# Performance work log

Hardware: AMD Instinct MI355X
Metric: run time of the kernel (lower is better)

Reference implementation:

```python
import jax, jax.numpy as jnp
import numpy as np

N = 100_000      # nodes
E = 1_600_000    # edges (before self-loops)
IN_C = 500
HID = 128
OUT_C = 64
L = 8
ALPHA = 0.1
THETA = 0.5


def setup_inputs() -> dict:
    key = jax.random.key(0)
    ks = jax.random.split(key, 6)
    x = jax.random.normal(ks[0], (N, IN_C), dtype=jnp.float32)
    edge_index = jax.random.randint(ks[1], (2, E), 0, N, dtype=jnp.int32)
    s0 = 1.0 / np.sqrt(IN_C)
    W_in = jax.random.uniform(ks[2], (IN_C, HID), jnp.float32, -s0, s0)
    b_in = jnp.zeros((HID,), jnp.float32)
    sh = 1.0 / np.sqrt(HID)
    W_conv = jax.random.uniform(ks[3], (L, HID, HID), jnp.float32, -sh, sh)
    W_out = jax.random.uniform(ks[4], (HID, OUT_C), jnp.float32, -sh, sh)
    b_out = jnp.zeros((OUT_C,), jnp.float32)
    return {"x": x, "edge_index": edge_index, "W_in": W_in, "b_in": b_in,
            "W_conv": W_conv, "W_out": W_out, "b_out": b_out}


def reference(x, edge_index, W_in, b_in, W_conv, W_out, b_out):
    # dropout is identity in eval mode
    loop = jnp.arange(N, dtype=edge_index.dtype)
    src = jnp.concatenate([edge_index[0], loop])  # add self-loops (gcn_norm)
    dst = jnp.concatenate([edge_index[1], loop])
    deg = jax.ops.segment_sum(jnp.ones_like(src, dtype=x.dtype), dst, num_segments=N)
    dinv = jnp.where(deg > 0, jax.lax.rsqrt(deg), 0.0)
    norm = dinv[src] * dinv[dst]  # symmetric normalization coeffs per edge

    h = jax.nn.relu(x @ W_in + b_in)
    h0 = h  # initial residual
    for l in range(L):
        beta = float(np.log(THETA / (l + 1) + 1.0))
        agg = jax.ops.segment_sum(h[src] * norm[:, None], dst, num_segments=N)  # Ahat @ h
        z = (1.0 - ALPHA) * agg + ALPHA * h0
        h = jax.nn.relu((1.0 - beta) * z + beta * (z @ W_conv[l]))
    return h @ W_out + b_out
```

## Files before the change

kernel.cpp:

```cpp
#include <hip/hip_runtime.h>
#include <hip/hip_fp16.h>
#include <cmath>

#define NN 100000
#define EE 1600000
#define INC 500
#define HIDC 128
#define OUTC 64
#define NLAYER 8
#define NW32 3125
#define GEMM_BLKS 782
#define FILL_BLKS 6250
#define FUSE_BLKS 7032

typedef float f32x4 __attribute__((ext_vector_type(4)));
typedef __bf16 bf16x8 __attribute__((ext_vector_type(8)));
typedef _Float16 f16x8 __attribute__((ext_vector_type(8)));
typedef short s16x4 __attribute__((ext_vector_type(4)));
typedef short s16x8 __attribute__((ext_vector_type(8)));

__device__ __forceinline__ unsigned short f2bf_rn(float f) {
  unsigned u = __float_as_uint(f);
  unsigned r = u + 0x7fffu + ((u >> 16) & 1u);
  return (unsigned short)(r >> 16);
}
__device__ __forceinline__ float bf2f(unsigned short h) {
  return __uint_as_float(((unsigned)h) << 16);
}

__device__ __forceinline__ int fraddr(int row, int k, int Kp) {
  return (row >> 4) * (Kp * 16) + (k >> 3) * 128 + (row & 15) * 8 + (k & 7);
}


__global__ void k_count_deg(const int* __restrict__ dst, int* __restrict__ deg, int E) {
  int e = blockIdx.x * blockDim.x + threadIdx.x;
  if (e < E) atomicAdd(&deg[dst[e]], 1);
}

__global__ void k_scan_block_sums(const int* __restrict__ deg, int* __restrict__ bsum, int n) {
  __shared__ int sm[256];
  int i = blockIdx.x * 256 + threadIdx.x;
  int v = (i < n) ? deg[i] + 1 : 0;
  sm[threadIdx.x] = v;
  __syncthreads();
  for (int s = 128; s > 0; s >>= 1) {
    if (threadIdx.x < s) sm[threadIdx.x] += sm[threadIdx.x + s];
    __syncthreads();
  }
  if (threadIdx.x == 0) bsum[blockIdx.x] = sm[0];
}

__global__ void k_scan_partials(int* __restrict__ bsum, int nb) {
  __shared__ int sm[512];
  int t = threadIdx.x;
  sm[t] = (t < nb) ? bsum[t] : 0;
  __syncthreads();
  for (int s = 1; s < 512; s <<= 1) {
    int v = (t >= s) ? sm[t - s] : 0;
    __syncthreads();
    sm[t] += v;
    __syncthreads();
  }
  if (t < nb) bsum[t] = (t == 0) ? 0 : sm[t - 1];
}

__global__ void k_scan_final(const int* __restrict__ deg, const int* __restrict__ bsum,
                             int* __restrict__ row_ptr, int n) {
  __shared__ int sm[256];
  int i = blockIdx.x * 256 + threadIdx.x;
  int v = (i < n) ? deg[i] + 1 : 0;
  sm[threadIdx.x] = v;
  __syncthreads();
  for (int s = 1; s < 256; s <<= 1) {
    int u = (threadIdx.x >= s) ? sm[threadIdx.x - s] : 0;
    __syncthreads();
    sm[threadIdx.x] += u;
    __syncthreads();
  }
  if (i < n) row_ptr[i] = bsum[blockIdx.x] + sm[threadIdx.x] - v;
}

__global__ void k_init_rows(const int* __restrict__ deg, const int* __restrict__ row_ptr,
                            int* __restrict__ cursor, int* __restrict__ col,
                            float* __restrict__ dinv, int n) {
  int i = blockIdx.x * blockDim.x + threadIdx.x;
  if (i < n) {
    int rp = row_ptr[i];
    col[rp] = i;
    cursor[i] = rp + 1;
    dinv[i] = rsqrtf((float)(deg[i] + 1));
  }
}


__global__ void k_prep_wfin(const float* __restrict__ W, unsigned short* __restrict__ fh,
                            unsigned short* __restrict__ fl) {
  int i = blockIdx.x * 256 + threadIdx.x;
  if (i >= HIDC * 512) return;
  int n = i / 512, k = i % 512;
  float v = (k < INC) ? W[(size_t)k * HIDC + n] : 0.f;
  unsigned short h = f2bf_rn(v);
  unsigned short l = f2bf_rn(v - bf2f(h));
  int a = fraddr(n, k, 512);
  fh[a] = h;
  fl[a] = l;
}


__global__ void k_prep_wf16(const float* __restrict__ W, __half* __restrict__ f,
                            int K, int N, float idc, float ws) {
  int i = blockIdx.x * 256 + threadIdx.x;
  if (i >= N * K) return;
  int n = i / K, k = i % K;
  float v = ws * W[(size_t)k * N + n] + ((k == n) ? idc : 0.f);
  f[fraddr(n, k, K)] = __float2half(v);
}


__global__ void __launch_bounds__(256) k_fill_gemm(
    const int* __restrict__ src, const int* __restrict__ dst,
    int* __restrict__ cursor, int* __restrict__ col,
    const float* __restrict__ A, const unsigned short* __restrict__ Bfh,
    const unsigned short* __restrict__ Bfl, const float* __restrict__ bias,
    __half* __restrict__ C16u, __half* __restrict__ C16s,
    const float* __restrict__ dinv) {
  __shared__ __align__(16) unsigned short Ah[128 * 40];
  __shared__ __align__(16) unsigned short Al[128 * 40];
  int bid = blockIdx.x;
  int tid = threadIdx.x;

  if (bid % 9 != 0) {
    int fidx = bid - (bid / 9 + 1);
    int e = fidx * 256 + tid;
    if (e < EE) {
      int pos = atomicAdd(&cursor[dst[e]], 1);
      col[pos] = src[e];
    }
    return;
  }

  int blk = bid / 9;
  int wid = tid >> 6, lane = tid & 63;
  int wr = wid >> 1, wc = wid & 1;
  int lr = lane & 15, kg = lane >> 4;
  int row0 = blk * 128;

  f32x4 acc[4][4];
#pragma unroll
  for (int m = 0; m < 4; ++m)
#pragma unroll
    for (int n = 0; n < 4; ++n) acc[m][n] = {0.f, 0.f, 0.f, 0.f};

  float4 va[4];
  auto issue_loads = [&](int kt) {
#pragma unroll
    for (int p = 0; p < 4; ++p) {
      int idx = tid + p * 256;
      int r = idx >> 3, kq = idx & 7;
      int gr = row0 + r, gk = kt + kq * 4;
      va[p] = make_float4(0.f, 0.f, 0.f, 0.f);
      if (gr < NN && gk < INC) va[p] = *reinterpret_cast<const float4*>(&A[(size_t)gr * INC + gk]);
    }
  };

  issue_loads(0);
  for (int kt = 0; kt < 512; kt += 32) {
#pragma unroll
    for (int p = 0; p < 4; ++p) {
      int idx = tid + p * 256;
      int r = idx >> 3, kq = idx & 7;
      const float* vp = &va[p].x;
      s16x4 h4, l4;
#pragma unroll
      for (int e = 0; e < 4; ++e) {
        unsigned short h = f2bf_rn(vp[e]);
        h4[e] = (short)h;
        l4[e] = (short)f2bf_rn(vp[e] - bf2f(h));
      }
      *reinterpret_cast<s16x4*>(&Ah[r * 40 + kq * 4]) = h4;
      *reinterpret_cast<s16x4*>(&Al[r * 40 + kq * 4]) = l4;
    }
    __syncthreads();
    if (kt + 32 < 512) issue_loads(kt + 32);

    bf16x8 afh[4], afl[4];
#pragma unroll
    for (int m = 0; m < 4; ++m) {
      int r = wr * 64 + m * 16 + lr;
      afh[m] = *reinterpret_cast<const bf16x8*>(&Ah[r * 40 + kg * 8]);
      afl[m] = *reinterpret_cast<const bf16x8*>(&Al[r * 40 + kg * 8]);
    }
#pragma unroll
    for (int n = 0; n < 4; ++n) {
      size_t bb = (size_t)(wc * 4 + n) * 8192 + (size_t)(kt / 8 + kg) * 128 + lr * 8;
      bf16x8 bh = *reinterpret_cast<const bf16x8*>(&Bfh[bb]);
      bf16x8 bl = *reinterpret_cast<const bf16x8*>(&Bfl[bb]);
#pragma unroll
      for (int m = 0; m < 4; ++m) {
        acc[m][n] = __builtin_amdgcn_mfma_f32_16x16x32_bf16(afh[m], bh, acc[m][n], 0, 0, 0);
        acc[m][n] = __builtin_amdgcn_mfma_f32_16x16x32_bf16(afl[m], bh, acc[m][n], 0, 0, 0);
        acc[m][n] = __builtin_amdgcn_mfma_f32_16x16x32_bf16(afh[m], bl, acc[m][n], 0, 0, 0);
      }
    }
    __syncthreads();
  }

#pragma unroll
  for (int m = 0; m < 4; ++m) {
#pragma unroll
    for (int n = 0; n < 4; ++n) {
      int gc = wc * 64 + n * 16 + lr;
#pragma unroll
      for (int q = 0; q < 4; ++q) {
        int gr = row0 + wr * 64 + m * 16 + kg * 4 + q;
        if (gr < NN) {
          float v = fmaxf(acc[m][n][q] + bias[gc], 0.f);
          C16u[(size_t)gr * HIDC + gc] = __float2half(v);
          C16s[(size_t)gr * HIDC + gc] = __float2half(v * dinv[gr]);
        }
      }
    }
  }
}


__global__ void __launch_bounds__(256) k_agg(
    const __half* __restrict__ hs, const __half* __restrict__ h0u,
    __half* __restrict__ zf,
    const int* __restrict__ row_ptr, const int* __restrict__ deg,
    const int* __restrict__ col, const float* __restrict__ dinv) {
  int wid = (blockIdx.x * blockDim.x + threadIdx.x) >> 6;
  int lane = threadIdx.x & 63;
  if (wid >= NN) return;
  int g = lane >> 4;
  int fl = lane & 15;
  int start = row_ptr[wid];
  int cnt = deg[wid] + 1;
  int nch = (cnt + 3) >> 2;

  float acc[8];
#pragma unroll
  for (int j = 0; j < 8; ++j) acc[j] = 0.f;

  auto load_chunk = [&](int ch, s16x8& v, float& m) {
    int e = ch * 4 + g;
    bool valid = e < cnt;
    int c = col[start + (valid ? e : 0)];
    m = valid ? 1.f : 0.f;
    v = *reinterpret_cast<const s16x8*>(&hs[(size_t)c * HIDC + fl * 8]);
  };

  s16x8 curv; float curm;
  load_chunk(0, curv, curm);
  for (int ch = 0; ch < nch; ++ch) {
    s16x8 nv = {}; float nm = 0.f;
    if (ch + 1 < nch) load_chunk(ch + 1, nv, nm);
    const __half2* hp = reinterpret_cast<const __half2*>(&curv);
#pragma unroll
    for (int j = 0; j < 4; ++j) {
      float2 f = __half22float2(hp[j]);
      acc[2 * j]     = fmaf(curm, f.x, acc[2 * j]);
      acc[2 * j + 1] = fmaf(curm, f.y, acc[2 * j + 1]);
    }
    curv = nv; curm = nm;
  }

#pragma unroll
  for (int j = 0; j < 8; ++j) {
    acc[j] += __shfl_xor(acc[j], 16, 64);
    acc[j] += __shfl_xor(acc[j], 32, 64);
  }

  if (g == 0) {
    float dr = dinv[wid] * 0.9f;
    s16x8 r0 = *reinterpret_cast<const s16x8*>(&h0u[(size_t)wid * HIDC + fl * 8]);
    const __half2* r0p = reinterpret_cast<const __half2*>(&r0);
    f16x8 w;
#pragma unroll
    for (int j = 0; j < 4; ++j) {
      float2 f0 = __half22float2(r0p[j]);
      w[2 * j]     = (_Float16)fmaf(dr, acc[2 * j],     0.1f * f0.x);
      w[2 * j + 1] = (_Float16)fmaf(dr, acc[2 * j + 1], 0.1f * f0.y);
    }
    int base = (wid >> 4) * (HIDC * 16) + fl * 128 + (wid & 15) * 8;
    *reinterpret_cast<f16x8*>(&zf[base]) = w;
  }
}


template <int NOUT, int EPI>
__global__ void __launch_bounds__(256) k_fgemm16(
    const __half* __restrict__ Af, const __half* __restrict__ Bf,
    const float* __restrict__ bias, const float* __restrict__ dinv,
    __half* __restrict__ Cs, __half* __restrict__ Cff, float* __restrict__ Cf) {
  constexpr int NF = NOUT / 16;
  int wv = threadIdx.x >> 6, lane = threadIdx.x & 63;
  int lr = lane & 15, kg = lane >> 4;
  int w32 = blockIdx.x * 4 + wv;
  if (w32 >= NW32) return;
  int row0 = w32 * 32;

  f32x4 acc[2][NF];
#pragma unroll
  for (int m = 0; m < 2; ++m)
#pragma unroll
    for (int n = 0; n < NF; ++n) acc[m][n] = {0.f, 0.f, 0.f, 0.f};

  const __half* Ab = Af + (size_t)(w32 * 2) * 2048 + kg * 128 + lr * 8;
  const __half* Bb = Bf + kg * 128 + lr * 8;

  f16x8 a0 = *reinterpret_cast<const f16x8*>(Ab);
  f16x8 a1 = *reinterpret_cast<const f16x8*>(Ab + 2048);
#pragma unroll
  for (int kt = 0; kt < 4; ++kt) {
    f16x8 n0, n1;
    if (kt < 3) {
      n0 = *reinterpret_cast<const f16x8*>(Ab + (kt + 1) * 512);
      n1 = *reinterpret_cast<const f16x8*>(Ab + 2048 + (kt + 1) * 512);
    }
#pragma unroll
    for (int n = 0; n < NF; ++n) {
      f16x8 b = *reinterpret_cast<const f16x8*>(Bb + n * 2048 + kt * 512);
      acc[0][n] = __builtin_amdgcn_mfma_f32_16x16x32_f16(a0, b, acc[0][n], 0, 0, 0);
      acc[1][n] = __builtin_amdgcn_mfma_f32_16x16x32_f16(a1, b, acc[1][n], 0, 0, 0);
    }
    if (kt < 3) { a0 = n0; a1 = n1; }
  }

#pragma unroll
  for (int m = 0; m < 2; ++m) {
#pragma unroll
    for (int q = 0; q < 4; ++q) {
      int gr = row0 + m * 16 + kg * 4 + q;
      float dv = (EPI == 0) ? (dinv[gr]) : 0.f;
#pragma unroll
      for (int n = 0; n < NF; ++n) {
        int gc = n * 16 + lr;
        float v = acc[m][n][q];
        if (EPI == 0) {
          v = fmaxf(v, 0.f);
          Cs[(size_t)gr * NOUT + gc] = __float2half(v * dv);
        } else if (EPI == 1) {
          v = fmaxf(v, 0.f);
          Cff[fraddr(gr, gc, HIDC)] = __float2half(v);
        } else {
          Cf[(size_t)gr * NOUT + gc] = v + bias[gc];
        }
      }
    }
  }
}


extern "C" void kernel_launch(void* const* d_in, const int* in_sizes, int n_in,
                              void* d_out, int out_size, void* d_ws, size_t ws_size,
                              hipStream_t stream) {
  const float* x     = (const float*)d_in[0];
  const int*   ei    = (const int*)d_in[1];
  const float* W_in  = (const float*)d_in[2];
  const float* b_in  = (const float*)d_in[3];
  const float* W_cv  = (const float*)d_in[4];
  const float* W_out = (const float*)d_in[5];
  const float* b_out = (const float*)d_in[6];
  float* out = (float*)d_out;

  char* ws = (char*)d_ws;
  size_t off = 0;
  auto alloc = [&](size_t bytes) {
    char* p = ws + off;
    off = (off + bytes + 255) & ~(size_t)255;
    return p;
  };
  int*    deg     = (int*)alloc((size_t)NN * 4);
  int*    row_ptr = (int*)alloc((size_t)NN * 4);
  int*    cursor  = (int*)alloc((size_t)NN * 4);
  int*    bsum    = (int*)alloc(512 * 4);
  float*  dinv    = (float*)alloc((size_t)NN * 4);
  int*    col     = (int*)alloc((size_t)(EE + NN) * 4);
  __half* h016u   = (__half*)alloc((size_t)NN * HIDC * 2);
  __half* h016s   = (__half*)alloc((size_t)NN * HIDC * 2);
  __half* hsA     = (__half*)alloc((size_t)NN * HIDC * 2);
  __half* hsB     = (__half*)alloc((size_t)NN * HIDC * 2);
  __half* zf      = (__half*)alloc((size_t)NN * HIDC * 2);
  __half* hf      = (__half*)alloc((size_t)NN * HIDC * 2);
  __half* wcv16   = (__half*)alloc((size_t)NLAYER * HIDC * HIDC * 2);
  __half* wout16  = (__half*)alloc((size_t)OUTC * HIDC * 2);
  unsigned short* win_h = (unsigned short*)alloc((size_t)HIDC * 512 * 2);
  unsigned short* win_l = (unsigned short*)alloc((size_t)HIDC * 512 * 2);

  const int* srcp = ei;
  const int* dstp = ei + EE;

  hipMemsetAsync(deg, 0, (size_t)NN * 4, stream);
  k_count_deg<<<(EE + 255) / 256, 256, 0, stream>>>(dstp, deg, EE);
  int nb = (NN + 255) / 256;
  k_scan_block_sums<<<nb, 256, 0, stream>>>(deg, bsum, NN);
  k_scan_partials<<<1, 512, 0, stream>>>(bsum, nb);
  k_scan_final<<<nb, 256, 0, stream>>>(deg, bsum, row_ptr, NN);
  k_init_rows<<<(NN + 255) / 256, 256, 0, stream>>>(deg, row_ptr, cursor, col, dinv, NN);

  k_prep_wfin<<<(HIDC * 512 + 255) / 256, 256, 0, stream>>>(W_in, win_h, win_l);
  for (int l = 0; l < NLAYER; ++l) {
    float beta = logf(0.5f / (float)(l + 1) + 1.0f);
    k_prep_wf16<<<(HIDC * HIDC + 255) / 256, 256, 0, stream>>>(
        W_cv + (size_t)l * HIDC * HIDC, wcv16 + (size_t)l * HIDC * HIDC,
        HIDC, HIDC, 1.0f - beta, beta);
  }
  k_prep_wf16<<<(OUTC * HIDC + 255) / 256, 256, 0, stream>>>(W_out, wout16, HIDC, OUTC,
                                                             0.f, 1.f);

  k_fill_gemm<<<FUSE_BLKS, 256, 0, stream>>>(srcp, dstp, cursor, col,
                                             x, win_h, win_l, b_in,
                                             h016u, h016s, dinv);

  int fgrid = (NW32 + 3) / 4;
  const __half* hcur = h016s;
  for (int l = 0; l < NLAYER; ++l) {
    k_agg<<<((size_t)NN * 64 + 255) / 256, 256, 0, stream>>>(hcur, h016u, zf,
                                                             row_ptr, deg, col, dinv);
    const __half* wl = wcv16 + (size_t)l * HIDC * HIDC;
    if (l < NLAYER - 1) {
      __half* tgt = (l & 1) ? hsB : hsA;
      k_fgemm16<128, 0><<<fgrid, 256, 0, stream>>>(zf, wl, nullptr, dinv,
                                                   tgt, nullptr, nullptr);
      hcur = tgt;
    } else {
      k_fgemm16<128, 1><<<fgrid, 256, 0, stream>>>(zf, wl, nullptr, nullptr,
                                                   nullptr, hf, nullptr);
    }
  }
  k_fgemm16<64, 2><<<fgrid, 256, 0, stream>>>(hf, wout16, b_out, nullptr,
                                              nullptr, nullptr, out);
}
```

Before: 1.093 ms.

## Fuse per-layer SpMM aggregation with the dense GEMM via LDS tile

Merges the aggregation kernel and the per-layer 128x128 GEMM into one kernel. Each wave aggregates 16 nodes serially into a swizzled LDS tile, then runs MFMA on that tile. This drops the zf round trip through global memory and one launch per layer. The cost is that each wave processes 16 nodes one after another instead of one node per wave, which lowers parallelism and latency hiding for the gather-bound aggregation.

Measured after the change: 1.415 ms. 29.5% more time.

```diff
diff --git a/kernel.cpp b/kernel.cpp
--- a/kernel.cpp
+++ b/kernel.cpp
@@ -9,8 +9,7 @@
 #define OUTC 64
 #define NLAYER 8
 #define NW32 3125
-#define GEMM_BLKS 782
-#define FILL_BLKS 6250
+#define NW16 6250
 #define FUSE_BLKS 7032
 
 typedef float f32x4 __attribute__((ext_vector_type(4)));
@@ -225,76 +224,119 @@
 }
 
 
-__global__ void __launch_bounds__(256) k_agg(
+template <int EPI>
+__global__ void __launch_bounds__(256) k_layer(
     const __half* __restrict__ hs, const __half* __restrict__ h0u,
-    __half* __restrict__ zf,
+    const __half* __restrict__ Bf,
     const int* __restrict__ row_ptr, const int* __restrict__ deg,
-    const int* __restrict__ col, const float* __restrict__ dinv) {
-  int wid = (blockIdx.x * blockDim.x + threadIdx.x) >> 6;
-  int lane = threadIdx.x & 63;
-  if (wid >= NN) return;
+    const int* __restrict__ col, const float* __restrict__ dinv,
+    __half* __restrict__ Cs, __half* __restrict__ Cff) {
+  __shared__ __half zbuf[4][16 * 128];
+  int wv = threadIdx.x >> 6, lane = threadIdx.x & 63;
+  int w16 = blockIdx.x * 4 + wv;
+  bool act = (w16 < NW16);
   int g = lane >> 4;
   int fl = lane & 15;
-  int start = row_ptr[wid];
-  int cnt = deg[wid] + 1;
-  int nch = (cnt + 3) >> 2;
-
-  float acc[8];
-#pragma unroll
-  for (int j = 0; j < 8; ++j) acc[j] = 0.f;
-
-  auto load_chunk = [&](int ch, s16x8& v, float& m) {
-    int e = ch * 4 + g;
-    bool valid = e < cnt;
-    int c = col[start + (valid ? e : 0)];
-    m = valid ? 1.f : 0.f;
-    v = *reinterpret_cast<const s16x8*>(&hs[(size_t)c * HIDC + fl * 8]);
-  };
-
-  s16x8 curv; float curm;
-  load_chunk(0, curv, curm);
-  for (int ch = 0; ch < nch; ++ch) {
-    s16x8 nv = {}; float nm = 0.f;
-    if (ch + 1 < nch) load_chunk(ch + 1, nv, nm);
-    const __half2* hp = reinterpret_cast<const __half2*>(&curv);
-#pragma unroll
-    for (int j = 0; j < 4; ++j) {
-      float2 f = __half22float2(hp[j]);
-      acc[2 * j]     = fmaf(curm, f.x, acc[2 * j]);
-      acc[2 * j + 1] = fmaf(curm, f.y, acc[2 * j + 1]);
-    }
-    curv = nv; curm = nm;
-  }
-
-#pragma unroll
-  for (int j = 0; j < 8; ++j) {
-    acc[j] += __shfl_xor(acc[j], 16, 64);
-    acc[j] += __shfl_xor(acc[j], 32, 64);
-  }
-
-  if (g == 0) {
-    float dr = dinv[wid] * 0.9f;
-    s16x8 r0 = *reinterpret_cast<const s16x8*>(&h0u[(size_t)wid * HIDC + fl * 8]);
-    const __half2* r0p = reinterpret_cast<const __half2*>(&r0);
-    f16x8 w;
-#pragma unroll
-    for (int j = 0; j < 4; ++j) {
-      float2 f0 = __half22float2(r0p[j]);
-      w[2 * j]     = (_Float16)fmaf(dr, acc[2 * j],     0.1f * f0.x);
-      w[2 * j + 1] = (_Float16)fmaf(dr, acc[2 * j + 1], 0.1f * f0.y);
-    }
-    int base = (wid >> 4) * (HIDC * 16) + fl * 128 + (wid & 15) * 8;
-    *reinterpret_cast<f16x8*>(&zf[base]) = w;
-  }
-}
-
-
-template <int NOUT, int EPI>
-__global__ void __launch_bounds__(256) k_fgemm16(
+  int row0 = w16 * 16;
+  __half* zb = zbuf[wv];
+
+  if (act) {
+    for (int r = 0; r < 16; ++r) {
+      int node = row0 + r;
+      int start = row_ptr[node];
+      int cnt = deg[node] + 1;
+      int nch = (cnt + 3) >> 2;
+
+      float acc[8];
+#pragma unroll
+      for (int j = 0; j < 8; ++j) acc[j] = 0.f;
+
+      auto load_chunk = [&](int ch, s16x8& v, float& m) {
+        int e = ch * 4 + g;
+        bool valid = e < cnt;
+        int c = col[start + (valid ? e : 0)];
+        m = valid ? 1.f : 0.f;
+        v = *reinterpret_cast<const s16x8*>(&hs[(size_t)c * HIDC + fl * 8]);
+      };
+
+      s16x8 curv; float curm;
+      load_chunk(0, curv, curm);
+      for (int ch = 0; ch < nch; ++ch) {
+        s16x8 nv = {}; float nm = 0.f;
+        if (ch + 1 < nch) load_chunk(ch + 1, nv, nm);
+        const __half2* hp = reinterpret_cast<const __half2*>(&curv);
+#pragma unroll
+        for (int j = 0; j < 4; ++j) {
+          float2 f = __half22float2(hp[j]);
+          acc[2 * j]     = fmaf(curm, f.x, acc[2 * j]);
+          acc[2 * j + 1] = fmaf(curm, f.y, acc[2 * j + 1]);
+        }
+        curv = nv; curm = nm;
+      }
+
+#pragma unroll
+      for (int j = 0; j < 8; ++j) {
+        acc[j] += __shfl_xor(acc[j], 16, 64);
+        acc[j] += __shfl_xor(acc[j], 32, 64);
+      }
+
+      if (g == 0) {
+        float dr = dinv[node] * 0.9f;
+        s16x8 r0 = *reinterpret_cast<const s16x8*>(&h0u[(size_t)node * HIDC + fl * 8]);
+        const __half2* r0p = reinterpret_cast<const __half2*>(&r0);
+        f16x8 w;
+#pragma unroll
+        for (int j = 0; j < 4; ++j) {
+          float2 f0 = __half22float2(r0p[j]);
+          w[2 * j]     = (_Float16)fmaf(dr, acc[2 * j],     0.1f * f0.x);
+          w[2 * j + 1] = (_Float16)fmaf(dr, acc[2 * j + 1], 0.1f * f0.y);
+        }
+        *reinterpret_cast<f16x8*>(&zb[r * 128 + ((fl * 8) ^ ((r & 7) << 3))]) = w;
+      }
+    }
+  }
+  __syncthreads();
+  if (!act) return;
+
+  int lr = lane & 15, kg = lane >> 4;
+  f32x4 acc[8];
+#pragma unroll
+  for (int n = 0; n < 8; ++n) acc[n] = {0.f, 0.f, 0.f, 0.f};
+
+  const __half* Bb = Bf + kg * 128 + lr * 8;
+#pragma unroll
+  for (int kt = 0; kt < 4; ++kt) {
+    f16x8 a = *reinterpret_cast<const f16x8*>(
+        &zb[lr * 128 + ((kt * 32 + kg * 8) ^ ((lr & 7) << 3))]);
+#pragma unroll
+    for (int n = 0; n < 8; ++n) {
+      f16x8 b = *reinterpret_cast<const f16x8*>(Bb + n * 2048 + kt * 512);
+      acc[n] = __builtin_amdgcn_mfma_f32_16x16x32_f16(a, b, acc[n], 0, 0, 0);
+    }
+  }
+
+#pragma unroll
+  for (int q = 0; q < 4; ++q) {
+    int gr = row0 + kg * 4 + q;
+    float dv = (EPI == 0) ? dinv[gr] : 0.f;
+#pragma unroll
+    for (int n = 0; n < 8; ++n) {
+      int gc = n * 16 + lr;
+      float v = fmaxf(acc[n][q], 0.f);
+      if (EPI == 0) {
+        Cs[(size_t)gr * HIDC + gc] = __float2half(v * dv);
+      } else {
+        Cff[fraddr(gr, gc, HIDC)] = __float2half(v);
+      }
+    }
+  }
+}
+
+
+__global__ void __launch_bounds__(256) k_fgemm_out(
     const __half* __restrict__ Af, const __half* __restrict__ Bf,
-    const float* __restrict__ bias, const float* __restrict__ dinv,
-    __half* __restrict__ Cs, __half* __restrict__ Cff, float* __restrict__ Cf) {
-  constexpr int NF = NOUT / 16;
+    const float* __restrict__ bias, float* __restrict__ Cf) {
+  constexpr int NF = OUTC / 16;
   int wv = threadIdx.x >> 6, lane = threadIdx.x & 63;
   int lr = lane & 15, kg = lane >> 4;
   int w32 = blockIdx.x * 4 + wv;
@@ -310,22 +352,16 @@
   const __half* Ab = Af + (size_t)(w32 * 2) * 2048 + kg * 128 + lr * 8;
   const __half* Bb = Bf + kg * 128 + lr * 8;
 
-  f16x8 a0 = *reinterpret_cast<const f16x8*>(Ab);
-  f16x8 a1 = *reinterpret_cast<const f16x8*>(Ab + 2048);
 #pragma unroll
   for (int kt = 0; kt < 4; ++kt) {
-    f16x8 n0, n1;
-    if (kt < 3) {
-      n0 = *reinterpret_cast<const f16x8*>(Ab + (kt + 1) * 512);
-      n1 = *reinterpret_cast<const f16x8*>(Ab + 2048 + (kt + 1) * 512);
-    }
+    f16x8 a0 = *reinterpret_cast<const f16x8*>(Ab + kt * 512);
+    f16x8 a1 = *reinterpret_cast<const f16x8*>(Ab + 2048 + kt * 512);
 #pragma unroll
     for (int n = 0; n < NF; ++n) {
       f16x8 b = *reinterpret_cast<const f16x8*>(Bb + n * 2048 + kt * 512);
       acc[0][n] = __builtin_amdgcn_mfma_f32_16x16x32_f16(a0, b, acc[0][n], 0, 0, 0);
       acc[1][n] = __builtin_amdgcn_mfma_f32_16x16x32_f16(a1, b, acc[1][n], 0, 0, 0);
     }
-    if (kt < 3) { a0 = n0; a1 = n1; }
   }
 
 #pragma unroll
@@ -333,20 +369,10 @@
 #pragma unroll
     for (int q = 0; q < 4; ++q) {
       int gr = row0 + m * 16 + kg * 4 + q;
-      float dv = (EPI == 0) ? (dinv[gr]) : 0.f;
 #pragma unroll
       for (int n = 0; n < NF; ++n) {
         int gc = n * 16 + lr;
-        float v = acc[m][n][q];
-        if (EPI == 0) {
-          v = fmaxf(v, 0.f);
-          Cs[(size_t)gr * NOUT + gc] = __float2half(v * dv);
-        } else if (EPI == 1) {
-          v = fmaxf(v, 0.f);
-          Cff[fraddr(gr, gc, HIDC)] = __float2half(v);
-        } else {
-          Cf[(size_t)gr * NOUT + gc] = v + bias[gc];
-        }
+        Cf[(size_t)gr * OUTC + gc] = acc[m][n][q] + bias[gc];
       }
     }
   }
@@ -382,7 +408,6 @@
   __half* h016s   = (__half*)alloc((size_t)NN * HIDC * 2);
   __half* hsA     = (__half*)alloc((size_t)NN * HIDC * 2);
   __half* hsB     = (__half*)alloc((size_t)NN * HIDC * 2);
-  __half* zf      = (__half*)alloc((size_t)NN * HIDC * 2);
   __half* hf      = (__half*)alloc((size_t)NN * HIDC * 2);
   __half* wcv16   = (__half*)alloc((size_t)NLAYER * HIDC * HIDC * 2);
   __half* wout16  = (__half*)alloc((size_t)OUTC * HIDC * 2);
@@ -414,22 +439,19 @@
                                              x, win_h, win_l, b_in,
                                              h016u, h016s, dinv);
 
-  int fgrid = (NW32 + 3) / 4;
+  int lgrid = (NW16 + 3) / 4;
   const __half* hcur = h016s;
   for (int l = 0; l < NLAYER; ++l) {
-    k_agg<<<((size_t)NN * 64 + 255) / 256, 256, 0, stream>>>(hcur, h016u, zf,
-                                                             row_ptr, deg, col, dinv);
     const __half* wl = wcv16 + (size_t)l * HIDC * HIDC;
     if (l < NLAYER - 1) {
       __half* tgt = (l & 1) ? hsB : hsA;
-      k_fgemm16<128, 0><<<fgrid, 256, 0, stream>>>(zf, wl, nullptr, dinv,
-                                                   tgt, nullptr, nullptr);
+      k_layer<0><<<lgrid, 256, 0, stream>>>(hcur, h016u, wl, row_ptr, deg, col, dinv,
+                                            tgt, nullptr);
       hcur = tgt;
     } else {
-      k_fgemm16<128, 1><<<fgrid, 256, 0, stream>>>(zf, wl, nullptr, nullptr,
-                                                   nullptr, hf, nullptr);
-    }
-  }
-  k_fgemm16<64, 2><<<fgrid, 256, 0, stream>>>(hf, wout16, b_out, nullptr,
-                                              nullptr, nullptr, out);
-}
+      k_layer<1><<<lgrid, 256, 0, stream>>>(hcur, h016u, wl, row_ptr, deg, col, dinv,
+                                            nullptr, hf);
+    }
+  }
+  k_fgemm_out<<<(NW32 + 3) / 4, 256, 0, stream>>>(hf, wout16, b_out, out);
+}
```
